# Optimization experiments

Measured on AMD Instinct MI355X. Metric: run time of the kernel, lower is better.

Reference implementation:

```python
import jax, jax.numpy as jnp
import numpy as np

IN_CH, OUT_CH, IN_W, K, PAD = 64, 64, 2048, 3, 1
OUT_W = IN_W + 2 * PAD - K + 1  # 2048


def setup_inputs() -> dict:
    key = jax.random.key(0)
    k1, k2, k3 = jax.random.split(key, 3)
    x = jax.random.normal(k1, (32, IN_CH, IN_W), dtype=jnp.float32)
    weights = jax.random.normal(k2, (OUT_W, OUT_CH, IN_CH, K), dtype=jnp.float32)
    bias = jax.random.normal(k3, (OUT_CH, OUT_W), dtype=jnp.float32)
    return {"x": x, "weights": weights, "bias": bias}


def reference(x, weights, bias):
    # x: (B, IC, W); weights: (OW, OC, IC, K); bias: (OC, OW)
    xp = jnp.pad(x, ((0, 0), (0, 0), (PAD, PAD)))  # (B, IC, W+2p)
    # Gather sliding windows: patches[b, ic, w, k] = xp[b, ic, w + k]
    idx = jnp.arange(OUT_W)[:, None] + jnp.arange(K)[None, :]  # (OW, K)
    patches = xp[:, :, idx]  # (B, IC, OW, K)
    # Per-position unshared contraction over (ic, k)
    out = jnp.einsum('bcwk,wock->bow', patches, weights)  # (B, OC, OW)
    return out + bias[None, :, :]
```

## Files before the change

### kernel.cpp

```cpp
#include <hip/hip_runtime.h>

typedef _Float16 f16x8 __attribute__((ext_vector_type(8)));
typedef float f32x4 __attribute__((ext_vector_type(4)));

#define IN_CH   64
#define OUT_CH  64
#define W_TOT   2048
#define KW      3
#define B_TOT   32
#define CK      192
#define LDST    200

static __device__ __forceinline__ f16x8 cvt8(const float4& a, const float4& b) {
    f16x8 r;
    r[0] = (_Float16)a.x; r[1] = (_Float16)a.y; r[2] = (_Float16)a.z; r[3] = (_Float16)a.w;
    r[4] = (_Float16)b.x; r[5] = (_Float16)b.y; r[6] = (_Float16)b.z; r[7] = (_Float16)b.w;
    return r;
}

__global__ __launch_bounds__(256, 5)
void lc1d_kernel(const float* __restrict__ x,
                 const float* __restrict__ wts,
                 const float* __restrict__ bias,
                 float* __restrict__ out) {
    __shared__ _Float16 Xp[B_TOT * LDST];

    const int tid = threadIdx.x;
    const int bid = blockIdx.x;
    const int w = (bid & 7) * 256 + (bid >> 3);

    const int lane = tid & 63;
    const int wv   = tid >> 6;
    const int l15  = lane & 15;
    const int kg   = lane >> 4;

    float xv[8][3];
    #pragma unroll
    for (int j = 0; j < 8; ++j) {
        const float* row = x + (size_t)(tid + 256 * j) * W_TOT;
        if (w == 0) {
            float2 lo = *reinterpret_cast<const float2*>(row);
            xv[j][0] = 0.f;  xv[j][1] = lo.x; xv[j][2] = lo.y;
        } else if (w == W_TOT - 1) {
            float2 lo = *reinterpret_cast<const float2*>(row + W_TOT - 2);
            xv[j][0] = lo.x; xv[j][1] = lo.y; xv[j][2] = 0.f;
        } else if ((w - 1) & 1) {
            float2 lo = *reinterpret_cast<const float2*>(row + (w - 1 - 1));
            float2 hi = *reinterpret_cast<const float2*>(row + (w - 1 + 1));
            xv[j][0] = lo.y; xv[j][1] = hi.x; xv[j][2] = hi.y;
        } else {
            float2 lo = *reinterpret_cast<const float2*>(row + (w - 1));
            float2 hi = *reinterpret_cast<const float2*>(row + (w + 1));
            xv[j][0] = lo.x; xv[j][1] = lo.y; xv[j][2] = hi.x;
        }
    }

    const int o = wv * 16 + l15;
    const float* wsrc = wts + (size_t)w * (OUT_CH * CK) + o * CK + kg * 8;
    float4 wf[6][2];
    #pragma unroll
    for (int ks = 0; ks < 6; ++ks) {
        wf[ks][0] = *reinterpret_cast<const float4*>(wsrc + ks * 32);
        wf[ks][1] = *reinterpret_cast<const float4*>(wsrc + ks * 32 + 4);
    }

    const float bv = bias[o * W_TOT + w];

    #pragma unroll
    for (int j = 0; j < 8; ++j) {
        int p = tid + 256 * j;
        int b = p >> 6;
        int c = p & 63;
        _Float16* dst = &Xp[b * LDST + c * 3];
        dst[0] = (_Float16)xv[j][0];
        dst[1] = (_Float16)xv[j][1];
        dst[2] = (_Float16)xv[j][2];
    }

    f16x8 bw[6];
    #pragma unroll
    for (int ks = 0; ks < 6; ++ks) bw[ks] = cvt8(wf[ks][0], wf[ks][1]);

    __syncthreads();

    const _Float16* Xb = &Xp[l15 * LDST + kg * 8];
    f32x4 acc0 = {0.f, 0.f, 0.f, 0.f};
    f32x4 acc1 = {0.f, 0.f, 0.f, 0.f};
    #pragma unroll
    for (int ks = 0; ks < 6; ++ks) {
        f16x8 a0 = *reinterpret_cast<const f16x8*>(Xb + ks * 32);
        f16x8 a1 = *reinterpret_cast<const f16x8*>(Xb + 16 * LDST + ks * 32);
        acc0 = __builtin_amdgcn_mfma_f32_16x16x32_f16(a0, bw[ks], acc0, 0, 0, 0);
        acc1 = __builtin_amdgcn_mfma_f32_16x16x32_f16(a1, bw[ks], acc1, 0, 0, 0);
    }

    #pragma unroll
    for (int r = 0; r < 4; ++r) {
        int b0 = kg * 4 + r;
        out[((size_t)(b0 * OUT_CH + o)) * W_TOT + w] = acc0[r] + bv;
        int b1 = 16 + kg * 4 + r;
        out[((size_t)(b1 * OUT_CH + o)) * W_TOT + w] = acc1[r] + bv;
    }
}

extern "C" void kernel_launch(void* const* d_in, const int* in_sizes, int n_in,
                              void* d_out, int out_size, void* d_ws, size_t ws_size,
                              hipStream_t stream) {
    const float* x    = (const float*)d_in[0];
    const float* wts  = (const float*)d_in[1];
    const float* bias = (const float*)d_in[2];
    float* out = (float*)d_out;
    hipLaunchKernelGGL(lc1d_kernel, dim3(2048), dim3(256), 0, stream,
                       x, wts, bias, out);
}
```

Baseline: 207.7 us.

## Stream per-position weights into LDS via async global_load_lds with XOR swizzle

Each block's 48 KB weight slice is no longer loaded into registers with float4 loads. It is now copied straight into shared memory using global_load_lds direct-to-LDS transfers, and an XOR swizzle on the row offset avoids bank conflicts when the fragments are read back. The weights are then read from LDS and converted to f16 per k-step inside the MFMA loop. This frees registers and lets the weight fetch overlap the x gather, at the cost of a much larger LDS footprint, which caps occupancy at 2 blocks per CU, and extra LDS reads.

```diff
diff --git a/kernel.cpp b/kernel.cpp
--- a/kernel.cpp
+++ b/kernel.cpp
@@ -1,4 +1,5 @@
 #include <hip/hip_runtime.h>
+#include <stdint.h>
 
 typedef _Float16 f16x8 __attribute__((ext_vector_type(8)));
 typedef float f32x4 __attribute__((ext_vector_type(4)));
@@ -9,30 +10,44 @@
 #define KW      3
 #define B_TOT   32
 #define CK      192
-#define LDST    200
+#define XPST    200
 
-static __device__ __forceinline__ f16x8 cvt8(const float4& a, const float4& b) {
+static __device__ __forceinline__ f16x8 cvt8(f32x4 a, f32x4 b) {
     f16x8 r;
-    r[0] = (_Float16)a.x; r[1] = (_Float16)a.y; r[2] = (_Float16)a.z; r[3] = (_Float16)a.w;
-    r[4] = (_Float16)b.x; r[5] = (_Float16)b.y; r[6] = (_Float16)b.z; r[7] = (_Float16)b.w;
+    r[0] = (_Float16)a[0]; r[1] = (_Float16)a[1]; r[2] = (_Float16)a[2]; r[3] = (_Float16)a[3];
+    r[4] = (_Float16)b[0]; r[5] = (_Float16)b[1]; r[6] = (_Float16)b[2]; r[7] = (_Float16)b[3];
     return r;
 }
 
-__global__ __launch_bounds__(256, 5)
+__global__ __launch_bounds__(256, 2)
 void lc1d_kernel(const float* __restrict__ x,
                  const float* __restrict__ wts,
                  const float* __restrict__ bias,
                  float* __restrict__ out) {
-    __shared__ _Float16 Xp[B_TOT * LDST];
+    __shared__ float    Wb[OUT_CH * CK];
+    __shared__ _Float16 Xp[B_TOT * XPST];
 
-    const int tid = threadIdx.x;
-    const int bid = blockIdx.x;
-    const int w = (bid & 7) * 256 + (bid >> 3);
-
+    const int tid  = threadIdx.x;
+    const int bid  = blockIdx.x;
+    const int w    = (bid & 7) * 256 + (bid >> 3);
     const int lane = tid & 63;
     const int wv   = tid >> 6;
     const int l15  = lane & 15;
     const int kg   = lane >> 4;
+
+    {
+        const char* wbase = (const char*)(wts + (size_t)w * (OUT_CH * CK));
+        #pragma unroll
+        for (int i = 0; i < 12; ++i) {
+            int d   = wv * 12288 + i * 1024 + lane * 16;
+            int o   = d / 768;
+            int src = d ^ ((o & 7) << 4);
+            __builtin_amdgcn_global_load_lds(
+                (const __attribute__((address_space(1))) uint32_t*)(wbase + src),
+                (__attribute__((address_space(3))) uint32_t*)((char*)Wb + wv * 12288 + i * 1024),
+                16, 0, 0);
+        }
+    }
 
     float xv[8][3];
     #pragma unroll
@@ -45,8 +60,8 @@
             float2 lo = *reinterpret_cast<const float2*>(row + W_TOT - 2);
             xv[j][0] = lo.x; xv[j][1] = lo.y; xv[j][2] = 0.f;
         } else if ((w - 1) & 1) {
-            float2 lo = *reinterpret_cast<const float2*>(row + (w - 1 - 1));
-            float2 hi = *reinterpret_cast<const float2*>(row + (w - 1 + 1));
+            float2 lo = *reinterpret_cast<const float2*>(row + (w - 2));
+            float2 hi = *reinterpret_cast<const float2*>(row + w);
             xv[j][0] = lo.y; xv[j][1] = hi.x; xv[j][2] = hi.y;
         } else {
             float2 lo = *reinterpret_cast<const float2*>(row + (w - 1));
@@ -56,42 +71,35 @@
     }
 
     const int o = wv * 16 + l15;
-    const float* wsrc = wts + (size_t)w * (OUT_CH * CK) + o * CK + kg * 8;
-    float4 wf[6][2];
-    #pragma unroll
-    for (int ks = 0; ks < 6; ++ks) {
-        wf[ks][0] = *reinterpret_cast<const float4*>(wsrc + ks * 32);
-        wf[ks][1] = *reinterpret_cast<const float4*>(wsrc + ks * 32 + 4);
-    }
-
     const float bv = bias[o * W_TOT + w];
 
     #pragma unroll
     for (int j = 0; j < 8; ++j) {
         int p = tid + 256 * j;
-        int b = p >> 6;
-        int c = p & 63;
-        _Float16* dst = &Xp[b * LDST + c * 3];
+        _Float16* dst = &Xp[(p >> 6) * XPST + (p & 63) * 3];
         dst[0] = (_Float16)xv[j][0];
         dst[1] = (_Float16)xv[j][1];
         dst[2] = (_Float16)xv[j][2];
     }
 
-    f16x8 bw[6];
-    #pragma unroll
-    for (int ks = 0; ks < 6; ++ks) bw[ks] = cvt8(wf[ks][0], wf[ks][1]);
-
     __syncthreads();
 
-    const _Float16* Xb = &Xp[l15 * LDST + kg * 8];
+    const _Float16* Xb   = &Xp[l15 * XPST + kg * 8];
+    const char*     wrow = (const char*)Wb + o * 768;
+    const int       sm   = (o & 7) << 4;
+
     f32x4 acc0 = {0.f, 0.f, 0.f, 0.f};
     f32x4 acc1 = {0.f, 0.f, 0.f, 0.f};
     #pragma unroll
     for (int ks = 0; ks < 6; ++ks) {
+        int Cb = ks * 128 + kg * 32;
+        f32x4 b0 = *reinterpret_cast<const f32x4*>(wrow + (Cb ^ sm));
+        f32x4 b1 = *reinterpret_cast<const f32x4*>(wrow + ((Cb + 16) ^ sm));
+        f16x8 bw = cvt8(b0, b1);
         f16x8 a0 = *reinterpret_cast<const f16x8*>(Xb + ks * 32);
-        f16x8 a1 = *reinterpret_cast<const f16x8*>(Xb + 16 * LDST + ks * 32);
-        acc0 = __builtin_amdgcn_mfma_f32_16x16x32_f16(a0, bw[ks], acc0, 0, 0, 0);
-        acc1 = __builtin_amdgcn_mfma_f32_16x16x32_f16(a1, bw[ks], acc1, 0, 0, 0);
+        f16x8 a1 = *reinterpret_cast<const f16x8*>(Xb + 16 * XPST + ks * 32);
+        acc0 = __builtin_amdgcn_mfma_f32_16x16x32_f16(a0, bw, acc0, 0, 0, 0);
+        acc1 = __builtin_amdgcn_mfma_f32_16x16x32_f16(a1, bw, acc1, 0, 0, 0);
     }
 
     #pragma unroll
```

Result: faster. 196.2 us (-5.5%).
